# Optimization experiments

Measured on AMD Instinct MI355X. Metric: run time of the kernel, lower is better.

The kernel has to match this reference:

```python
import jax, jax.numpy as jnp
import numpy as np

N, E, G = 50000, 400000, 64   # nodes, edges, graphs
HEADS = 4
F_IN, H1, C3, OUT = 64, 96, 64, 10  # in feats, hidden (3*32), last conv out, classes


def seg_softmax(alpha, index, num_segments):
    # numerically stable softmax over segments (PyG softmax(alpha, edge_index_i))
    amax = jax.ops.segment_max(alpha, index, num_segments)
    amax = jnp.where(jnp.isfinite(amax), amax, 0.0)
    e = jnp.exp(alpha - amax[index])
    denom = jax.ops.segment_sum(e, index, num_segments)
    return e / (denom[index] + 1e-16)


def general_conv(x, src, dst, Wm, bm, att, Ws=None, bs=None):
    # GeneralConv (attention=True, additive, directed_msg, aggr='add')
    C = att.shape[-1]
    m = (x[src] @ Wm + bm).reshape(-1, HEADS, C)              # [E,H,C] gathered messages
    a = jax.nn.leaky_relu((m * att).sum(-1), 0.2)             # [E,H] attention logits
    a = seg_softmax(a, dst, N)                                # segment softmax per dest node
    agg = jax.ops.segment_sum(m * a[..., None], dst, N)       # [N,H,C] scatter-add
    out = agg.mean(axis=1)                                    # head mean -> [N,C]
    if Ws is None:                                            # lin_self = Identity (in==out)
        return out + x
    return out + x @ Ws + bs


def setup_inputs():
    key = jax.random.key(0)
    ks = jax.random.split(key, 16)
    s = 0.05
    return {
        "x": jax.random.normal(ks[0], (N, F_IN), jnp.float32),
        "edge_index": jax.random.randint(ks[1], (2, E), 0, N, jnp.int32),
        "batch": jnp.sort(jax.random.randint(ks[2], (N,), 0, G, jnp.int32)),
        # layer 1: F_IN -> H1
        "Wm1": jax.random.normal(ks[3], (F_IN, HEADS * H1), jnp.float32) * s,
        "bm1": jnp.zeros((HEADS * H1,), jnp.float32),
        "att1": jax.random.normal(ks[4], (HEADS, H1), jnp.float32) * s,
        "Ws1": jax.random.normal(ks[5], (F_IN, H1), jnp.float32) * s,
        "bs1": jnp.zeros((H1,), jnp.float32),
        # layer 2: H1 -> H1 (lin_self = Identity)
        "Wm2": jax.random.normal(ks[6], (H1, HEADS * H1), jnp.float32) * s,
        "bm2": jnp.zeros((HEADS * H1,), jnp.float32),
        "att2": jax.random.normal(ks[7], (HEADS, H1), jnp.float32) * s,
        # layer 3: H1 -> C3
        "Wm3": jax.random.normal(ks[8], (H1, HEADS * C3), jnp.float32) * s,
        "bm3": jnp.zeros((HEADS * C3,), jnp.float32),
        "att3": jax.random.normal(ks[9], (HEADS, C3), jnp.float32) * s,
        "Ws3": jax.random.normal(ks[10], (H1, C3), jnp.float32) * s,
        "bs3": jnp.zeros((C3,), jnp.float32),
        # classifier
        "Wfc": jax.random.normal(ks[11], (C3, OUT), jnp.float32) * s,
        "bfc": jnp.zeros((OUT,), jnp.float32),
    }


def reference(x, edge_index, batch, Wm1, bm1, att1, Ws1, bs1,
              Wm2, bm2, att2, Wm3, bm3, att3, Ws3, bs3, Wfc, bfc):
    src, dst = edge_index[0], edge_index[1]
    h = general_conv(x, src, dst, Wm1, bm1, att1, Ws1, bs1)
    h = general_conv(h, src, dst, Wm2, bm2, att2)
    h = general_conv(h, src, dst, Wm3, bm3, att3, Ws3, bs3)
    # global_mean_pool
    ssum = jax.ops.segment_sum(h, batch, G)
    cnt = jax.ops.segment_sum(jnp.ones((N, 1), h.dtype), batch, G)
    pooled = ssum / jnp.maximum(cnt, 1.0)                      # [G,C3]
    logits = pooled @ Wfc + bfc
    return jax.nn.log_softmax(logits, axis=1)
```

## Files before the change

### kernel.cpp

```cpp
#include <hip/hip_runtime.h>
#include <hip/hip_bf16.h>
#include <stdint.h>

using bf16 = __hip_bfloat16;
typedef __attribute__((ext_vector_type(8))) short bf16x8;
typedef __attribute__((ext_vector_type(4))) float f32x4;
typedef __attribute__((ext_vector_type(2))) float f32x2;

#define NN 50000
#define NE 400000
#define NG 64
#define NHEADS 4
#define FIN 64
#define HID 96
#define CC3 64
#define NOUT 10

#define SCAN_BLOCK 256
#define NPART ((NN + SCAN_BLOCK - 1) / SCAN_BLOCK)
#define GB16 ((NN/16 + 3) / 4)

__device__ __forceinline__ float b2f(bf16 h){ return __bfloat162float(h); }
__device__ __forceinline__ bf16 f2b(float f){ return __float2bfloat16(f); }

#define NTJOBS 5
struct PrepJobs {
  const float* W[NTJOBS]; bf16* WT[NTJOBS]; int K[NTJOBS]; int Nc[NTJOBS];
  const float* LWm[3]; const float* Latt[3]; const float* Lbm[3];
  bf16* LWT[3]; int LK[3]; int LC[3]; int LncMain[3];
  float* lb;
  int* deg; float* psum; int* done;
};
__global__ __launch_bounds__(256) void prep_kernel(PrepJobs j){
  int bid = blockIdx.x;
  if (bid < 3){
    int l = bid;
    const float* Wm = j.LWm[l]; const float* att = j.Latt[l]; const float* bm = j.Lbm[l];
    bf16* WT = j.LWT[l];
    int K = j.LK[l], C = j.LC[l], ncMain = j.LncMain[l];
    for (int idx = threadIdx.x; idx < K*4; idx += 256){
      int k = idx >> 2, h = idx & 3;
      float a = 0.f;
      for (int c=0;c<C;++c) a += Wm[(size_t)k*(4*C) + h*C + c] * att[h*C + c];
      WT[(size_t)(ncMain+h)*K + k] = f2b(a);
    }
    for (int idx = threadIdx.x; idx < 12*K; idx += 256){
      int col = ncMain + 4 + idx / K, k = idx % K;
      WT[(size_t)col*K + k] = f2b(0.f);
    }
    if (threadIdx.x < 4){
      int h = threadIdx.x; float a = 0.f;
      for (int c=0;c<C;++c) a += bm[h*C + c] * att[h*C + c];
      j.lb[l*4 + h] = a;
    }
  } else if (bid < 3 + 256){
    int b = bid - 3;
    for (int t=0; t<NTJOBS; ++t){
      int K = j.K[t], Nc = j.Nc[t], total = K*Nc;
      for (int i = b*256 + threadIdx.x; i < total; i += 256*256){
        int k = i / Nc, n = i % Nc;
        j.WT[t][(size_t)n*K + k] = f2b(j.W[t][i]);
      }
    }
  } else if (bid < 3 + 256 + NPART){
    int i = (bid - 3 - 256)*256 + threadIdx.x;
    if (i < NN) j.deg[i] = 0;
  } else {
    for (int i = threadIdx.x; i < NG*CC3; i += 256) j.psum[i] = 0.f;
    if (threadIdx.x == 0) *j.done = 0;
  }
}

__global__ void deg_kernel(const int* __restrict__ ei, int* __restrict__ deg){
  int e = blockIdx.x*256 + threadIdx.x;
  if (e < NE) atomicAdd(&deg[ei[NE + e]], 1);
}

__global__ __launch_bounds__(256) void scan_part_kernel(const int* __restrict__ deg,
    int* __restrict__ partials, int* __restrict__ done, int* __restrict__ off){
  __shared__ int ws[4];
  __shared__ int lastflag;
  __shared__ int buf[256];
  int i = blockIdx.x*SCAN_BLOCK + threadIdx.x;
  int v = (i < NN) ? deg[i] : 0;
  int lane = threadIdx.x & 63, w = threadIdx.x >> 6;
  int s = v;
  #pragma unroll
  for (int m=1;m<64;m<<=1) s += __shfl_xor(s,m);
  if (lane==0) ws[w]=s;
  __syncthreads();
  if (threadIdx.x==0){
    int tot = ws[0]+ws[1]+ws[2]+ws[3];
    atomicExch(&partials[blockIdx.x], tot);
    __threadfence();
    int old = atomicAdd(done, 1);
    lastflag = (old == NPART-1) ? 1 : 0;
  }
  __syncthreads();
  if (lastflag){
    int t = threadIdx.x;
    int pv = (t < NPART) ? atomicAdd(&partials[t], 0) : 0;
    buf[t] = pv; __syncthreads();
    for (int st=1; st<256; st<<=1){
      int x = (t>=st) ? buf[t-st] : 0;
      __syncthreads();
      buf[t] += x;
      __syncthreads();
    }
    if (t < NPART) atomicExch(&partials[t], buf[t] - pv);
    if (t == 0) off[NN] = buf[255];
  }
}

__global__ __launch_bounds__(256) void scan_final_kernel(const int* __restrict__ deg,
    const int* __restrict__ partials, int* __restrict__ off, int* __restrict__ cursor){
  __shared__ int buf[256];
  int i = blockIdx.x*SCAN_BLOCK + threadIdx.x;
  int t = threadIdx.x;
  int v = (i<NN) ? deg[i] : 0;
  buf[t] = v; __syncthreads();
  for (int s=1;s<256;s<<=1){
    int x = (t>=s) ? buf[t-s] : 0;
    __syncthreads();
    buf[t] += x;
    __syncthreads();
  }
  int ex = partials[blockIdx.x] + buf[t] - v;
  if (i<NN){ off[i]=ex; cursor[i]=ex; }
}

__global__ void scatter_kernel(const int* __restrict__ ei, int* __restrict__ cursor,
                               int* __restrict__ csr_src){
  int e = blockIdx.x*256 + threadIdx.x;
  if (e < NE){
    int d = ei[NE + e];
    int slot = atomicAdd(&cursor[d], 1);
    csr_src[slot] = ei[e];
  }
}

template<int K, bool F32A>
__global__ __launch_bounds__(256) void gemm_mfma(const void* __restrict__ Ap,
    const bf16* __restrict__ WT, const float* __restrict__ biasMain,
    const float* __restrict__ lb4, uint8_t* __restrict__ outMain, int ncMain,
    float* __restrict__ EL, const float* __restrict__ biasSelf,
    bf16* __restrict__ outSelf, int ncSelf, int msgG, int totalU, int UPB)
{
  constexpr int KT = K/32;
  __shared__ unsigned int sbuf[4][16][16];
  const int wave = threadIdx.x >> 6, lane = threadIdx.x & 63;
  const int tile = blockIdx.x*4 + wave;
  if (tile >= NN/16) return;
  const int lm = lane & 15, q = lane >> 4;
  const int nodeRow = tile*16 + lm;
  const int rdRow = lane >> 2, rdCol = lane & 3;
  const int outRow = tile*16 + rdRow;

  bf16x8 xfrag[KT];
  if (F32A){
    const float* Af = (const float*)Ap;
    #pragma unroll
    for (int kt=0; kt<KT; ++kt){
      float4 a0 = *(const float4*)(Af + (size_t)nodeRow*K + kt*32 + q*8);
      float4 a1 = *(const float4*)(Af + (size_t)nodeRow*K + kt*32 + q*8 + 4);
      bf16 tmp[8];
      tmp[0]=f2b(a0.x); tmp[1]=f2b(a0.y); tmp[2]=f2b(a0.z); tmp[3]=f2b(a0.w);
      tmp[4]=f2b(a1.x); tmp[5]=f2b(a1.y); tmp[6]=f2b(a1.z); tmp[7]=f2b(a1.w);
      xfrag[kt] = *(const bf16x8*)tmp;
    }
  } else {
    const bf16* A = (const bf16*)Ap;
    #pragma unroll
    for (int kt=0; kt<KT; ++kt)
      xfrag[kt] = *(const bf16x8*)(A + (size_t)nodeRow*K + kt*32 + q*8);
  }

  const int u0 = blockIdx.y*UPB, u1 = min(u0+UPB, totalU);
  for (int u=u0; u<u1; ++u){
    if (u < msgG){
      #pragma unroll
      for (int t=0;t<4;++t){
        int ct = u*4 + t;
        f32x4 acc = {};
        #pragma unroll
        for (int kt=0; kt<KT; ++kt){
          bf16x8 wfrag = *(const bf16x8*)(WT + (size_t)(ct*16+lm)*K + kt*32 + q*8);
          acc = __builtin_amdgcn_mfma_f32_16x16x32_bf16(wfrag, xfrag[kt], acc, 0,0,0);
        }
        int wc = ct*16 + q*4;
        float v0 = acc[0]+biasMain[wc],   v1 = acc[1]+biasMain[wc+1];
        float v2 = acc[2]+biasMain[wc+2], v3 = acc[3]+biasMain[wc+3];
        int pk = 0;
        pk = __builtin_amdgcn_cvt_pk_fp8_f32(v0, v1, pk, false);
        pk = __builtin_amdgcn_cvt_pk_fp8_f32(v2, v3, pk, true);
        sbuf[wave][lm][t*4 + q] = (unsigned int)pk;
      }
      __builtin_amdgcn_wave_barrier();
      uint4 v = *(uint4*)&sbuf[wave][rdRow][rdCol*4];
      *(uint4*)(outMain + (size_t)outRow*ncMain + u*64 + rdCol*16) = v;
      __builtin_amdgcn_wave_barrier();
    } else if (u == msgG){
      int ct = ncMain/16;
      f32x4 acc = {};
      #pragma unroll
      for (int kt=0; kt<KT; ++kt){
        bf16x8 wfrag = *(const bf16x8*)(WT + (size_t)(ct*16+lm)*K + kt*32 + q*8);
        acc = __builtin_amdgcn_mfma_f32_16x16x32_bf16(wfrag, xfrag[kt], acc, 0,0,0);
      }
      if (q == 0){
        float4 e;
        float l;
        l = acc[0]+lb4[0]; l = (l>=0.f)?l:0.2f*l; e.x = __expf(fminf(fmaxf(l,-60.f),60.f));
        l = acc[1]+lb4[1]; l = (l>=0.f)?l:0.2f*l; e.y = __expf(fminf(fmaxf(l,-60.f),60.f));
        l = acc[2]+lb4[2]; l = (l>=0.f)?l:0.2f*l; e.z = __expf(fminf(fmaxf(l,-60.f),60.f));
        l = acc[3]+lb4[3]; l = (l>=0.f)?l:0.2f*l; e.w = __expf(fminf(fmaxf(l,-60.f),60.f));
        *(float4*)(EL + 4*(size_t)nodeRow) = e;
      }
    } else {
      int sg = u - msgG - 1;
      #pragma unroll
      for (int t=0;t<2;++t){
        int ct = ncMain/16 + 1 + sg*2 + t;
        f32x4 acc = {};
        #pragma unroll
        for (int kt=0; kt<KT; ++kt){
          bf16x8 wfrag = *(const bf16x8*)(WT + (size_t)(ct*16+lm)*K + kt*32 + q*8);
          acc = __builtin_amdgcn_mfma_f32_16x16x32_bf16(wfrag, xfrag[kt], acc, 0,0,0);
        }
        int c = ct*16 + q*4 - ncMain - 16;
        bf16 st[4];
        st[0]=f2b(acc[0]+biasSelf[c]);   st[1]=f2b(acc[1]+biasSelf[c+1]);
        st[2]=f2b(acc[2]+biasSelf[c+2]); st[3]=f2b(acc[3]+biasSelf[c+3]);
        uint2 uu = *(uint2*)st;
        sbuf[wave][lm][t*8 + q*2]     = uu.x;
        sbuf[wave][lm][t*8 + q*2 + 1] = uu.y;
      }
      __builtin_amdgcn_wave_barrier();
      uint4 v = *(uint4*)&sbuf[wave][rdRow][rdCol*4];
      *(uint4*)(outSelf + (size_t)outRow*ncSelf + sg*32 + rdCol*8) = v;
      __builtin_amdgcn_wave_barrier();
    }
  }
}

template<int C, bool FP>
__global__ __launch_bounds__(256) void conv_agg(const int* __restrict__ off,
    const int* __restrict__ csr_src, const float* __restrict__ EL,
    const uint8_t* __restrict__ M8, const bf16* __restrict__ Hself,
    bf16* __restrict__ Hout, const int* __restrict__ batch, float* __restrict__ psum)
{
  constexpr int R = 4*C;
  __shared__ float red[4][R];
  const int wave = threadIdx.x >> 6, lane = threadIdx.x & 63;
  const int n = blockIdx.x*4 + wave;
  const int e0 = off[n], e1 = off[n+1];

  const bool active = (8*lane) < R;
  const int hidx = min(3, (8*lane) / C);
  const int myoff = active ? lane*8 : 0;
  float acc[8] = {0,0,0,0,0,0,0,0};
  float dnl = 0.f;

  for (int base=e0; base<e1; base+=8){
    const int cnt8 = min(8, e1-base);
    int sreg = (lane < cnt8) ? csr_src[base+lane] : 0;
    int sv[8];
    #pragma unroll
    for (int j=0;j<8;++j) sv[j] = __shfl(sreg, j);

    float wl[8]; uint2 u[8];
    #pragma unroll
    for (int j=0;j<8;++j){
      wl[j] = EL[4*(size_t)sv[j] + hidx];
      u[j]  = *(const uint2*)(M8 + (size_t)sv[j]*R + myoff);
    }
    #pragma unroll
    for (int j=0;j<8;++j){
      float w = (j < cnt8) ? wl[j] : 0.f;
      dnl += w;
      f32x2 a0 = __builtin_amdgcn_cvt_pk_f32_fp8((int)u[j].x, false);
      f32x2 a1 = __builtin_amdgcn_cvt_pk_f32_fp8((int)u[j].x, true);
      f32x2 a2 = __builtin_amdgcn_cvt_pk_f32_fp8((int)u[j].y, false);
      f32x2 a3 = __builtin_amdgcn_cvt_pk_f32_fp8((int)u[j].y, true);
      acc[0] += a0.x*w;  acc[1] += a0.y*w;
      acc[2] += a1.x*w;  acc[3] += a1.y*w;
      acc[4] += a2.x*w;  acc[5] += a2.y*w;
      acc[6] += a3.x*w;  acc[7] += a3.y*w;
    }
  }

  float rd = 1.f/(dnl + 1e-16f);
  if (active){
    #pragma unroll
    for (int j=0;j<8;++j) red[wave][8*lane+j] = acc[j]*rd;
  }
  __syncthreads();

  if (!FP){
    for (int c=lane; c<C; c+=64){
      float v = 0.25f*(red[wave][c] + red[wave][C+c] + red[wave][2*C+c] + red[wave][3*C+c]);
      Hout[(size_t)n*C + c] = f2b(v + b2f(Hself[(size_t)n*C + c]));
    }
  } else {
    if (wave == 0){
      int c = lane;
      int nb0 = blockIdx.x*4;
      int curg = batch[nb0];
      float a = 0.f;
      #pragma unroll
      for (int i=0;i<4;++i){
        float v = 0.25f*(red[i][c] + red[i][C+c] + red[i][2*C+c] + red[i][3*C+c]);
        v += b2f(Hself[(size_t)(nb0+i)*C + c]);
        int g = batch[nb0+i];
        if (g != curg){ atomicAdd(&psum[curg*C + c], a); a = 0.f; curg = g; }
        a += v;
      }
      atomicAdd(&psum[curg*C + c], a);
    }
  }
}

__global__ __launch_bounds__(64) void fc_kernel(const float* __restrict__ psum,
    const int* __restrict__ batch, const float* __restrict__ Wfc,
    const float* __restrict__ bfc, float* __restrict__ out){
  int g = blockIdx.x, t = threadIdx.x;
  __shared__ int sb[2];
  if (t < 2){
    int target = g + t;
    int lo=0, hi=NN;
    while (lo<hi){ int mid=(lo+hi)>>1; if (batch[mid]<target) lo=mid+1; else hi=mid; }
    sb[t]=lo;
  }
  __syncthreads();
  float cnt = (float)(sb[1]-sb[0]);
  __shared__ float p[CC3];
  __shared__ float lg[NOUT];
  p[t] = psum[g*CC3 + t] / fmaxf(cnt, 1.0f);
  __syncthreads();
  if (t < NOUT){
    float a = bfc[t];
    for (int c=0;c<CC3;++c) a += p[c]*Wfc[c*NOUT + t];
    lg[t] = a;
  }
  __syncthreads();
  if (t < NOUT){
    float m = -INFINITY;
    #pragma unroll
    for (int i=0;i<NOUT;++i) m = fmaxf(m, lg[i]);
    float s = 0.f;
    #pragma unroll
    for (int i=0;i<NOUT;++i) s += __expf(lg[i]-m);
    out[g*NOUT + t] = lg[t] - m - __logf(s);
  }
}

extern "C" void kernel_launch(void* const* d_in, const int* in_sizes, int n_in,
                              void* d_out, int out_size, void* d_ws, size_t ws_size,
                              hipStream_t stream) {
  const float* xf    = (const float*)d_in[0];
  const int*   ei    = (const int*)d_in[1];
  const int*   batch = (const int*)d_in[2];
  const float* pWm1  = (const float*)d_in[3];
  const float* pbm1  = (const float*)d_in[4];
  const float* patt1 = (const float*)d_in[5];
  const float* pWs1  = (const float*)d_in[6];
  const float* pbs1  = (const float*)d_in[7];
  const float* pWm2  = (const float*)d_in[8];
  const float* pbm2  = (const float*)d_in[9];
  const float* patt2 = (const float*)d_in[10];
  const float* pWm3  = (const float*)d_in[11];
  const float* pbm3  = (const float*)d_in[12];
  const float* patt3 = (const float*)d_in[13];
  const float* pWs3  = (const float*)d_in[14];
  const float* pbs3  = (const float*)d_in[15];
  const float* pWfc  = (const float*)d_in[16];
  const float* pbfc  = (const float*)d_in[17];

  char* p = (char*)d_ws;
  auto alloc = [&](size_t bytes)->char*{ char* q = p; p += (bytes + 255) & ~(size_t)255; return q; };
  int*     deg     = (int*)  alloc(NN*sizeof(int));
  int*     off     = (int*)  alloc((NN+1)*sizeof(int));
  int*     cursor  = (int*)  alloc(NN*sizeof(int));
  int*     csr_src = (int*)  alloc(NE*sizeof(int));
  int*     partials= (int*)  alloc(NPART*sizeof(int));
  int*     done    = (int*)  alloc(sizeof(int));
  float*   EL      = (float*)alloc((size_t)NN*4*sizeof(float));
  uint8_t* Mb8     = (uint8_t*)alloc((size_t)NN*384);
  bf16*    H1b     = (bf16*) alloc((size_t)NN*96*sizeof(bf16));
  bf16*    H2b     = (bf16*) alloc((size_t)NN*96*sizeof(bf16));
  float*   psum    = (float*)alloc((size_t)NG*CC3*sizeof(float));
  bf16*  WT1cat = (bf16*)alloc((size_t)496*FIN*sizeof(bf16));
  bf16*  WT2cat = (bf16*)alloc((size_t)400*HID*sizeof(bf16));
  bf16*  WT3cat = (bf16*)alloc((size_t)336*HID*sizeof(bf16));
  float* lb     = (float*)alloc(12*sizeof(float));
  bf16*  H3b = H1b;

  PrepJobs pj;
  pj.W[0]=pWm1; pj.WT[0]=WT1cat;                 pj.K[0]=FIN; pj.Nc[0]=384;
  pj.W[1]=pWs1; pj.WT[1]=WT1cat+(size_t)400*FIN; pj.K[1]=FIN; pj.Nc[1]=96;
  pj.W[2]=pWm2; pj.WT[2]=WT2cat;                 pj.K[2]=HID; pj.Nc[2]=384;
  pj.W[3]=pWm3; pj.WT[3]=WT3cat;                 pj.K[3]=HID; pj.Nc[3]=256;
  pj.W[4]=pWs3; pj.WT[4]=WT3cat+(size_t)272*HID; pj.K[4]=HID; pj.Nc[4]=64;
  pj.LWm[0]=pWm1; pj.Latt[0]=patt1; pj.Lbm[0]=pbm1; pj.LWT[0]=WT1cat; pj.LK[0]=FIN; pj.LC[0]=96; pj.LncMain[0]=384;
  pj.LWm[1]=pWm2; pj.Latt[1]=patt2; pj.Lbm[1]=pbm2; pj.LWT[1]=WT2cat; pj.LK[1]=HID; pj.LC[1]=96; pj.LncMain[1]=384;
  pj.LWm[2]=pWm3; pj.Latt[2]=patt3; pj.Lbm[2]=pbm3; pj.LWT[2]=WT3cat; pj.LK[2]=HID; pj.LC[2]=64; pj.LncMain[2]=256;
  pj.lb = lb; pj.deg = deg; pj.psum = psum; pj.done = done;
  prep_kernel<<<3+256+NPART+1, 256, 0, stream>>>(pj);

  deg_kernel<<<(NE+255)/256, 256, 0, stream>>>(ei, deg);
  scan_part_kernel<<<NPART, 256, 0, stream>>>(deg, partials, done, off);
  scan_final_kernel<<<NPART, 256, 0, stream>>>(deg, partials, off, cursor);
  scatter_kernel<<<(NE+255)/256, 256, 0, stream>>>(ei, cursor, csr_src);

  const int AB = NN/4;

  gemm_mfma<64,true><<<dim3(GB16,4), 256, 0, stream>>>(xf, WT1cat, pbm1, lb,
                                                       Mb8, 384, EL, pbs1, H1b, 96,
                                                       6, 10, 3);
  conv_agg<96,false><<<AB, 256, 0, stream>>>(off, csr_src, EL, Mb8, H1b, H1b,
                                             batch, psum);
  gemm_mfma<96,false><<<dim3(GB16,4), 256, 0, stream>>>(H1b, WT2cat, pbm2, lb+4,
                                                        Mb8, 384, EL, pbm2, nullptr, 0,
                                                        6, 7, 2);
  conv_agg<96,false><<<AB, 256, 0, stream>>>(off, csr_src, EL, Mb8, H1b, H2b,
                                             batch, psum);
  gemm_mfma<96,false><<<dim3(GB16,3), 256, 0, stream>>>(H2b, WT3cat, pbm3, lb+8,
                                                        Mb8, 256, EL, pbs3, H3b, 64,
                                                        4, 7, 3);
  conv_agg<64,true><<<AB, 256, 0, stream>>>(off, csr_src, EL, Mb8, H3b, nullptr,
                                            batch, psum);

  fc_kernel<<<NG, 64, 0, stream>>>(psum, batch, pWfc, pbfc, (float*)d_out);
}
```

Baseline: 356.2 us.

## Aggregate raw features before the linear map and fuse the GEMM into aggregation

The linear message transform is moved past the attention-weighted aggregation. Each node first gathers bf16 neighbour features per head (4*K wide), and a single per-node GEMM then applies the head-averaged weights, the bias (through an indicator column), the self term, and the next layer's attention logits. This drops the per-layer fp8 message tensor (NN x 384) and the separate GEMM launches, and precomputes folded weight matrices in two prep kernels. The trade-off is a wider gather (bf16 source features per head) and a larger K in the fused GEMM, with rounding now happening at different points.

```diff
diff --git a/kernel.cpp b/kernel.cpp
--- a/kernel.cpp
+++ b/kernel.cpp
@@ -5,12 +5,10 @@
 using bf16 = __hip_bfloat16;
 typedef __attribute__((ext_vector_type(8))) short bf16x8;
 typedef __attribute__((ext_vector_type(4))) float f32x4;
-typedef __attribute__((ext_vector_type(2))) float f32x2;
 
 #define NN 50000
 #define NE 400000
 #define NG 64
-#define NHEADS 4
 #define FIN 64
 #define HID 96
 #define CC3 64
@@ -18,56 +16,105 @@
 
 #define SCAN_BLOCK 256
 #define NPART ((NN + SCAN_BLOCK - 1) / SCAN_BLOCK)
-#define GB16 ((NN/16 + 3) / 4)
 
 __device__ __forceinline__ float b2f(bf16 h){ return __bfloat162float(h); }
 __device__ __forceinline__ bf16 f2b(float f){ return __float2bfloat16(f); }
-
-#define NTJOBS 5
-struct PrepJobs {
-  const float* W[NTJOBS]; bf16* WT[NTJOBS]; int K[NTJOBS]; int Nc[NTJOBS];
-  const float* LWm[3]; const float* Latt[3]; const float* Lbm[3];
-  bf16* LWT[3]; int LK[3]; int LC[3]; int LncMain[3];
-  float* lb;
+__device__ __forceinline__ float bs2f(short s){
+  union { float f; unsigned int u; } c;
+  c.u = ((unsigned int)(unsigned short)s) << 16;
+  return c.f;
+}
+
+struct PrepA {
+  const float *Wm1,*att1,*bm1,*Wm2,*att2,*bm2,*Wm3,*att3,*bm3,*bs1;
+  float *f2,*f3,*lbv,*zb; bf16* WTf1;
   int* deg; float* psum; int* done;
 };
-__global__ __launch_bounds__(256) void prep_kernel(PrepJobs j){
+__global__ __launch_bounds__(256) void prep_a_kernel(PrepA j){
   int bid = blockIdx.x;
-  if (bid < 3){
-    int l = bid;
-    const float* Wm = j.LWm[l]; const float* att = j.Latt[l]; const float* bm = j.Lbm[l];
-    bf16* WT = j.LWT[l];
-    int K = j.LK[l], C = j.LC[l], ncMain = j.LncMain[l];
-    for (int idx = threadIdx.x; idx < K*4; idx += 256){
-      int k = idx >> 2, h = idx & 3;
-      float a = 0.f;
-      for (int c=0;c<C;++c) a += Wm[(size_t)k*(4*C) + h*C + c] * att[h*C + c];
-      WT[(size_t)(ncMain+h)*K + k] = f2b(a);
-    }
-    for (int idx = threadIdx.x; idx < 12*K; idx += 256){
-      int col = ncMain + 4 + idx / K, k = idx % K;
-      WT[(size_t)col*K + k] = f2b(0.f);
-    }
+  if (bid == 0){
+    for (int i=threadIdx.x; i<96*4; i+=256){
+      int k=i>>2, h=i&3; float a=0.f;
+      for (int c=0;c<96;++c) a += j.Wm2[k*384 + h*96 + c]*j.att2[h*96+c];
+      j.f2[i]=a;
+    }
+    for (int i=threadIdx.x; i<96*4; i+=256){
+      int k=i>>2, h=i&3; float a=0.f;
+      for (int c=0;c<64;++c) a += j.Wm3[k*256 + h*64 + c]*j.att3[h*64+c];
+      j.f3[i]=a;
+    }
+    for (int i=threadIdx.x; i<16*64; i+=256){
+      int col=i>>6, k=i&63; float a=0.f;
+      if (col<4){ for (int c=0;c<96;++c) a += j.Wm1[k*384 + col*96 + c]*j.att1[col*96+c]; }
+      j.WTf1[i] = f2b(a);
+    }
+    if (threadIdx.x < 96) j.zb[threadIdx.x] = 0.f;
+    __syncthreads();
     if (threadIdx.x < 4){
-      int h = threadIdx.x; float a = 0.f;
-      for (int c=0;c<C;++c) a += bm[h*C + c] * att[h*C + c];
-      j.lb[l*4 + h] = a;
-    }
-  } else if (bid < 3 + 256){
-    int b = bid - 3;
-    for (int t=0; t<NTJOBS; ++t){
-      int K = j.K[t], Nc = j.Nc[t], total = K*Nc;
-      for (int i = b*256 + threadIdx.x; i < total; i += 256*256){
-        int k = i / Nc, n = i % Nc;
-        j.WT[t][(size_t)n*K + k] = f2b(j.W[t][i]);
-      }
-    }
-  } else if (bid < 3 + 256 + NPART){
-    int i = (bid - 3 - 256)*256 + threadIdx.x;
-    if (i < NN) j.deg[i] = 0;
+      int h = threadIdx.x;
+      float l1=0.f,l2=0.f,l3=0.f;
+      for (int c=0;c<96;++c) l1 += j.bm1[h*96+c]*j.att1[h*96+c];
+      for (int c=0;c<96;++c) l2 += j.bm2[h*96+c]*j.att2[h*96+c];
+      for (int c=0;c<64;++c) l3 += j.bm3[h*64+c]*j.att3[h*64+c];
+      float e2 = l2;
+      for (int k=0;k<96;++k) e2 += j.bs1[k]*j.f2[k*4+h];
+      j.lbv[h]=l1; j.lbv[4+h]=e2; j.lbv[8+h]=l3;
+    }
+  } else if (bid <= NPART){
+    int i=(bid-1)*256+threadIdx.x;
+    if (i<NN) j.deg[i]=0;
   } else {
-    for (int i = threadIdx.x; i < NG*CC3; i += 256) j.psum[i] = 0.f;
-    if (threadIdx.x == 0) *j.done = 0;
+    for (int i=threadIdx.x; i<NG*CC3; i+=256) j.psum[i]=0.f;
+    if (threadIdx.x==0) *j.done = 0;
+  }
+}
+
+struct PrepB {
+  const float *Wm1,*bm1,*Ws1,*Wm2,*bm2,*Wm3,*bm3,*Ws3;
+  const float *f2,*f3;
+  bf16 *WT1,*WT2,*WT3;
+};
+__device__ __forceinline__ float w1full(const PrepB& j, int k, int c){
+  if (k < 256) return 0.25f*j.Wm1[(k&63)*384 + (k>>6)*96 + c];
+  if (k == 256) return 0.25f*(j.bm1[c]+j.bm1[96+c]+j.bm1[192+c]+j.bm1[288+c]);
+  if (k < 288) return 0.f;
+  return j.Ws1[(k-288)*96 + c];
+}
+__device__ __forceinline__ float w2full(const PrepB& j, int k, int c){
+  if (k < 384){ int kk=k%96, h=k/96; return 0.25f*j.Wm2[kk*384 + h*96 + c]; }
+  if (k == 384) return 0.25f*(j.bm2[c]+j.bm2[96+c]+j.bm2[192+c]+j.bm2[288+c]);
+  if (k < 416) return 0.f;
+  return (k-416==c) ? 1.f : 0.f;
+}
+__device__ __forceinline__ float w3full(const PrepB& j, int k, int c){
+  if (k < 384){ int kk=k%96, h=k/96; return 0.25f*j.Wm3[kk*256 + h*64 + c]; }
+  if (k == 384) return 0.25f*(j.bm3[c]+j.bm3[64+c]+j.bm3[128+c]+j.bm3[192+c]);
+  if (k < 416) return 0.f;
+  return j.Ws3[(k-416)*64 + c];
+}
+__global__ __launch_bounds__(256) void prep_b_kernel(PrepB j){
+  int idx = blockIdx.x*256 + threadIdx.x;
+  if (idx < 112*352){
+    int col = idx/352, k = idx - col*352;
+    float v;
+    if (col < 96) v = w1full(j,k,col);
+    else if (col < 100){ int h=col-96; float a=0.f;
+      for (int c=0;c<96;++c) a += w1full(j,k,c)*j.f2[c*4+h]; v=a; }
+    else v = 0.f;
+    j.WT1[col*352 + k] = f2b(v);
+  } else if (idx < 112*352 + 112*512){
+    int r = idx - 112*352;
+    int col = r/512, k = r - col*512;
+    float v;
+    if (col < 96) v = w2full(j,k,col);
+    else if (col < 100){ int h=col-96; float a=0.f;
+      for (int c=0;c<96;++c) a += w2full(j,k,c)*j.f3[c*4+h]; v=a; }
+    else v = 0.f;
+    j.WT2[col*512 + k] = f2b(v);
+  } else {
+    int r = idx - 112*352 - 112*512;
+    int col = r/512, k = r - col*512;
+    j.WT3[col*512 + k] = f2b(w3full(j,k,col));
   }
 }
 
@@ -139,183 +186,171 @@
   }
 }
 
-template<int K, bool F32A>
-__global__ __launch_bounds__(256) void gemm_mfma(const void* __restrict__ Ap,
-    const bf16* __restrict__ WT, const float* __restrict__ biasMain,
-    const float* __restrict__ lb4, uint8_t* __restrict__ outMain, int ncMain,
-    float* __restrict__ EL, const float* __restrict__ biasSelf,
-    bf16* __restrict__ outSelf, int ncSelf, int msgG, int totalU, int UPB)
+__global__ __launch_bounds__(256) void el1_kernel(const float* __restrict__ x,
+    const bf16* __restrict__ WTf1, const float* __restrict__ lbv,
+    bf16* __restrict__ xb, float* __restrict__ EL)
 {
-  constexpr int KT = K/32;
-  __shared__ unsigned int sbuf[4][16][16];
-  const int wave = threadIdx.x >> 6, lane = threadIdx.x & 63;
+  const int wave = threadIdx.x>>6, lane = threadIdx.x&63;
   const int tile = blockIdx.x*4 + wave;
   if (tile >= NN/16) return;
-  const int lm = lane & 15, q = lane >> 4;
-  const int nodeRow = tile*16 + lm;
-  const int rdRow = lane >> 2, rdCol = lane & 3;
-  const int outRow = tile*16 + rdRow;
-
-  bf16x8 xfrag[KT];
-  if (F32A){
-    const float* Af = (const float*)Ap;
+  const int lm = lane&15, q = lane>>4;
+  const size_t row = (size_t)tile*16 + lm;
+  bf16x8 xf[2];
+  #pragma unroll
+  for (int kt=0;kt<2;++kt){
+    float4 a0 = *(const float4*)(x + row*64 + kt*32 + q*8);
+    float4 a1 = *(const float4*)(x + row*64 + kt*32 + q*8 + 4);
+    bf16 t[8] = {f2b(a0.x),f2b(a0.y),f2b(a0.z),f2b(a0.w),
+                 f2b(a1.x),f2b(a1.y),f2b(a1.z),f2b(a1.w)};
+    xf[kt] = *(const bf16x8*)t;
+    *(bf16x8*)(xb + row*64 + kt*32 + q*8) = xf[kt];
+  }
+  f32x4 acc = {};
+  #pragma unroll
+  for (int kt=0;kt<2;++kt){
+    bf16x8 wf = *(const bf16x8*)(WTf1 + (size_t)lm*64 + kt*32 + q*8);
+    acc = __builtin_amdgcn_mfma_f32_16x16x32_bf16(wf, xf[kt], acc, 0,0,0);
+  }
+  if (q==0){
+    float4 e; float l;
+    l=acc[0]+lbv[0]; l=(l>=0.f)?l:0.2f*l; e.x=__expf(fminf(fmaxf(l,-60.f),60.f));
+    l=acc[1]+lbv[1]; l=(l>=0.f)?l:0.2f*l; e.y=__expf(fminf(fmaxf(l,-60.f),60.f));
+    l=acc[2]+lbv[2]; l=(l>=0.f)?l:0.2f*l; e.z=__expf(fminf(fmaxf(l,-60.f),60.f));
+    l=acc[3]+lbv[3]; l=(l>=0.f)?l:0.2f*l; e.w=__expf(fminf(fmaxf(l,-60.f),60.f));
+    *(float4*)(EL + 4*row) = e;
+  }
+}
+
+template<int KH, int NCT, bool POOL>
+__global__ __launch_bounds__(256) void conv_gemm(
+    const int* __restrict__ off, const int* __restrict__ csr_src,
+    const float* __restrict__ ELin, const bf16* __restrict__ Hprev,
+    const bf16* __restrict__ WT, const float* __restrict__ bias,
+    const float* __restrict__ lbe, bf16* __restrict__ Hout,
+    float* __restrict__ ELout, const int* __restrict__ batch,
+    float* __restrict__ psum)
+{
+  constexpr int R   = 4*KH;
+  constexpr int KS  = R + 32;
+  constexpr int KA  = KS + KH;
+  constexpr int KTS = KS/32, KTH = KH/32, KT = KA/32;
+  constexpr int SP  = (KS==288) ? 296 : 424;
+  constexpr int OB  = POOL ? (16*68*4) : (16*104*2);
+  __shared__ __align__(16) unsigned short Slds[16][SP];
+  __shared__ __align__(16) char obuf[OB];
+  __shared__ int sbat[16];
+
+  const int wave = threadIdx.x>>6, lane = threadIdx.x&63;
+  const int n0 = blockIdx.x*16;
+
+  if (POOL && threadIdx.x < 16) sbat[threadIdx.x] = batch[n0+threadIdx.x];
+
+  const bool act = (8*lane) < R;
+  const int h  = min((8*lane)/KH, 3);
+  const int kk = (8*lane) % KH;
+
+  int ofl = 0;
+  if (lane < 5) ofl = off[n0 + wave*4 + lane];
+
+  for (int i=0;i<4;++i){
+    const int e0 = __shfl(ofl, i), e1 = __shfl(ofl, i+1);
+    float acc[8] = {0.f,0.f,0.f,0.f,0.f,0.f,0.f,0.f};
+    float dnl = 0.f;
+    for (int base=e0; base<e1; base+=8){
+      const int cnt = min(8, e1-base);
+      int sreg = (lane < cnt) ? csr_src[base+lane] : 0;
+      int sv[8];
+      #pragma unroll
+      for (int jj=0;jj<8;++jj) sv[jj] = __shfl(sreg, jj);
+      float wl[8]; bf16x8 u[8];
+      #pragma unroll
+      for (int jj=0;jj<8;++jj){
+        wl[jj] = ELin[4*(size_t)sv[jj] + h];
+        u[jj]  = *(const bf16x8*)(Hprev + (size_t)sv[jj]*KH + kk);
+      }
+      #pragma unroll
+      for (int jj=0;jj<8;++jj){
+        float w = (jj < cnt) ? wl[jj] : 0.f;
+        dnl += w;
+        #pragma unroll
+        for (int t=0;t<8;++t) acc[t] += w * bs2f(u[jj][t]);
+      }
+    }
+    const float rd = 1.f/(dnl + 1e-16f);
+    const int srow = wave*4 + i;
+    if (act){
+      bf16 st[8];
+      #pragma unroll
+      for (int t=0;t<8;++t) st[t] = f2b(acc[t]*rd);
+      *(bf16x8*)&Slds[srow][8*lane] = *(const bf16x8*)st;
+    } else if (8*lane < KS){
+      bf16 st[8] = {};
+      if (8*lane == R) st[0] = f2b((e1 > e0) ? 1.f : 0.f);
+      *(bf16x8*)&Slds[srow][8*lane] = *(const bf16x8*)st;
+    }
+  }
+  __syncthreads();
+
+  const int lm = lane&15, q = lane>>4;
+  bf16x8 xf[KT];
+  #pragma unroll
+  for (int kt=0; kt<KTS; ++kt)
+    xf[kt] = *(const bf16x8*)&Slds[lm][kt*32 + q*8];
+  #pragma unroll
+  for (int kt=0; kt<KTH; ++kt)
+    xf[KTS+kt] = *(const bf16x8*)(Hprev + (size_t)(n0+lm)*KH + kt*32 + q*8);
+
+  for (int ct = wave; ct < NCT; ct += 4){
+    f32x4 acc = {};
     #pragma unroll
     for (int kt=0; kt<KT; ++kt){
-      float4 a0 = *(const float4*)(Af + (size_t)nodeRow*K + kt*32 + q*8);
-      float4 a1 = *(const float4*)(Af + (size_t)nodeRow*K + kt*32 + q*8 + 4);
-      bf16 tmp[8];
-      tmp[0]=f2b(a0.x); tmp[1]=f2b(a0.y); tmp[2]=f2b(a0.z); tmp[3]=f2b(a0.w);
-      tmp[4]=f2b(a1.x); tmp[5]=f2b(a1.y); tmp[6]=f2b(a1.z); tmp[7]=f2b(a1.w);
-      xfrag[kt] = *(const bf16x8*)tmp;
-    }
-  } else {
-    const bf16* A = (const bf16*)Ap;
-    #pragma unroll
-    for (int kt=0; kt<KT; ++kt)
-      xfrag[kt] = *(const bf16x8*)(A + (size_t)nodeRow*K + kt*32 + q*8);
-  }
-
-  const int u0 = blockIdx.y*UPB, u1 = min(u0+UPB, totalU);
-  for (int u=u0; u<u1; ++u){
-    if (u < msgG){
-      #pragma unroll
-      for (int t=0;t<4;++t){
-        int ct = u*4 + t;
-        f32x4 acc = {};
-        #pragma unroll
-        for (int kt=0; kt<KT; ++kt){
-          bf16x8 wfrag = *(const bf16x8*)(WT + (size_t)(ct*16+lm)*K + kt*32 + q*8);
-          acc = __builtin_amdgcn_mfma_f32_16x16x32_bf16(wfrag, xfrag[kt], acc, 0,0,0);
-        }
-        int wc = ct*16 + q*4;
-        float v0 = acc[0]+biasMain[wc],   v1 = acc[1]+biasMain[wc+1];
-        float v2 = acc[2]+biasMain[wc+2], v3 = acc[3]+biasMain[wc+3];
-        int pk = 0;
-        pk = __builtin_amdgcn_cvt_pk_fp8_f32(v0, v1, pk, false);
-        pk = __builtin_amdgcn_cvt_pk_fp8_f32(v2, v3, pk, true);
-        sbuf[wave][lm][t*4 + q] = (unsigned int)pk;
-      }
-      __builtin_amdgcn_wave_barrier();
-      uint4 v = *(uint4*)&sbuf[wave][rdRow][rdCol*4];
-      *(uint4*)(outMain + (size_t)outRow*ncMain + u*64 + rdCol*16) = v;
-      __builtin_amdgcn_wave_barrier();
-    } else if (u == msgG){
-      int ct = ncMain/16;
-      f32x4 acc = {};
-      #pragma unroll
-      for (int kt=0; kt<KT; ++kt){
-        bf16x8 wfrag = *(const bf16x8*)(WT + (size_t)(ct*16+lm)*K + kt*32 + q*8);
-        acc = __builtin_amdgcn_mfma_f32_16x16x32_bf16(wfrag, xfrag[kt], acc, 0,0,0);
-      }
+      bf16x8 wf = *(const bf16x8*)(WT + (size_t)(ct*16+lm)*KA + kt*32 + q*8);
+      acc = __builtin_amdgcn_mfma_f32_16x16x32_bf16(wf, xf[kt], acc, 0,0,0);
+    }
+    if (!POOL && ct == NCT-1){
       if (q == 0){
-        float4 e;
-        float l;
-        l = acc[0]+lb4[0]; l = (l>=0.f)?l:0.2f*l; e.x = __expf(fminf(fmaxf(l,-60.f),60.f));
-        l = acc[1]+lb4[1]; l = (l>=0.f)?l:0.2f*l; e.y = __expf(fminf(fmaxf(l,-60.f),60.f));
-        l = acc[2]+lb4[2]; l = (l>=0.f)?l:0.2f*l; e.z = __expf(fminf(fmaxf(l,-60.f),60.f));
-        l = acc[3]+lb4[3]; l = (l>=0.f)?l:0.2f*l; e.w = __expf(fminf(fmaxf(l,-60.f),60.f));
-        *(float4*)(EL + 4*(size_t)nodeRow) = e;
+        float4 e; float l;
+        l=acc[0]+lbe[0]; l=(l>=0.f)?l:0.2f*l; e.x=__expf(fminf(fmaxf(l,-60.f),60.f));
+        l=acc[1]+lbe[1]; l=(l>=0.f)?l:0.2f*l; e.y=__expf(fminf(fmaxf(l,-60.f),60.f));
+        l=acc[2]+lbe[2]; l=(l>=0.f)?l:0.2f*l; e.z=__expf(fminf(fmaxf(l,-60.f),60.f));
+        l=acc[3]+lbe[3]; l=(l>=0.f)?l:0.2f*l; e.w=__expf(fminf(fmaxf(l,-60.f),60.f));
+        *(float4*)(ELout + 4*(size_t)(n0+lm)) = e;
       }
     } else {
-      int sg = u - msgG - 1;
+      const int c = ct*16 + q*4;
+      if (POOL){
+        float* orow = (float*)obuf + lm*68;
+        orow[c]   = acc[0]+bias[c];   orow[c+1] = acc[1]+bias[c+1];
+        orow[c+2] = acc[2]+bias[c+2]; orow[c+3] = acc[3]+bias[c+3];
+      } else {
+        bf16 st[4] = {f2b(acc[0]+bias[c]),   f2b(acc[1]+bias[c+1]),
+                      f2b(acc[2]+bias[c+2]), f2b(acc[3]+bias[c+3])};
+        *(uint2*)((unsigned short*)obuf + lm*104 + c) = *(const uint2*)st;
+      }
+    }
+  }
+  __syncthreads();
+
+  if (!POOL){
+    const int t = threadIdx.x;
+    if (t < 192){
+      const int r = t/12, ch = t - r*12;
+      uint4 v = *(const uint4*)((const unsigned short*)obuf + r*104 + ch*8);
+      *(uint4*)(Hout + (size_t)(n0+r)*96 + ch*8) = v;
+    }
+  } else {
+    if (threadIdx.x < 64){
+      const float* ob = (const float*)obuf;
+      const int c = threadIdx.x;
+      int curg = sbat[0]; float a = 0.f;
       #pragma unroll
-      for (int t=0;t<2;++t){
-        int ct = ncMain/16 + 1 + sg*2 + t;
-        f32x4 acc = {};
-        #pragma unroll
-        for (int kt=0; kt<KT; ++kt){
-          bf16x8 wfrag = *(const bf16x8*)(WT + (size_t)(ct*16+lm)*K + kt*32 + q*8);
-          acc = __builtin_amdgcn_mfma_f32_16x16x32_bf16(wfrag, xfrag[kt], acc, 0,0,0);
-        }
-        int c = ct*16 + q*4 - ncMain - 16;
-        bf16 st[4];
-        st[0]=f2b(acc[0]+biasSelf[c]);   st[1]=f2b(acc[1]+biasSelf[c+1]);
-        st[2]=f2b(acc[2]+biasSelf[c+2]); st[3]=f2b(acc[3]+biasSelf[c+3]);
-        uint2 uu = *(uint2*)st;
-        sbuf[wave][lm][t*8 + q*2]     = uu.x;
-        sbuf[wave][lm][t*8 + q*2 + 1] = uu.y;
-      }
-      __builtin_amdgcn_wave_barrier();
-      uint4 v = *(uint4*)&sbuf[wave][rdRow][rdCol*4];
-      *(uint4*)(outSelf + (size_t)outRow*ncSelf + sg*32 + rdCol*8) = v;
-      __builtin_amdgcn_wave_barrier();
-    }
-  }
-}
-
-template<int C, bool FP>
-__global__ __launch_bounds__(256) void conv_agg(const int* __restrict__ off,
-    const int* __restrict__ csr_src, const float* __restrict__ EL,
-    const uint8_t* __restrict__ M8, const bf16* __restrict__ Hself,
-    bf16* __restrict__ Hout, const int* __restrict__ batch, float* __restrict__ psum)
-{
-  constexpr int R = 4*C;
-  __shared__ float red[4][R];
-  const int wave = threadIdx.x >> 6, lane = threadIdx.x & 63;
-  const int n = blockIdx.x*4 + wave;
-  const int e0 = off[n], e1 = off[n+1];
-
-  const bool active = (8*lane) < R;
-  const int hidx = min(3, (8*lane) / C);
-  const int myoff = active ? lane*8 : 0;
-  float acc[8] = {0,0,0,0,0,0,0,0};
-  float dnl = 0.f;
-
-  for (int base=e0; base<e1; base+=8){
-    const int cnt8 = min(8, e1-base);
-    int sreg = (lane < cnt8) ? csr_src[base+lane] : 0;
-    int sv[8];
-    #pragma unroll
-    for (int j=0;j<8;++j) sv[j] = __shfl(sreg, j);
-
-    float wl[8]; uint2 u[8];
-    #pragma unroll
-    for (int j=0;j<8;++j){
-      wl[j] = EL[4*(size_t)sv[j] + hidx];
-      u[j]  = *(const uint2*)(M8 + (size_t)sv[j]*R + myoff);
-    }
-    #pragma unroll
-    for (int j=0;j<8;++j){
-      float w = (j < cnt8) ? wl[j] : 0.f;
-      dnl += w;
-      f32x2 a0 = __builtin_amdgcn_cvt_pk_f32_fp8((int)u[j].x, false);
-      f32x2 a1 = __builtin_amdgcn_cvt_pk_f32_fp8((int)u[j].x, true);
-      f32x2 a2 = __builtin_amdgcn_cvt_pk_f32_fp8((int)u[j].y, false);
-      f32x2 a3 = __builtin_amdgcn_cvt_pk_f32_fp8((int)u[j].y, true);
-      acc[0] += a0.x*w;  acc[1] += a0.y*w;
-      acc[2] += a1.x*w;  acc[3] += a1.y*w;
-      acc[4] += a2.x*w;  acc[5] += a2.y*w;
-      acc[6] += a3.x*w;  acc[7] += a3.y*w;
-    }
-  }
-
-  float rd = 1.f/(dnl + 1e-16f);
-  if (active){
-    #pragma unroll
-    for (int j=0;j<8;++j) red[wave][8*lane+j] = acc[j]*rd;
-  }
-  __syncthreads();
-
-  if (!FP){
-    for (int c=lane; c<C; c+=64){
-      float v = 0.25f*(red[wave][c] + red[wave][C+c] + red[wave][2*C+c] + red[wave][3*C+c]);
-      Hout[(size_t)n*C + c] = f2b(v + b2f(Hself[(size_t)n*C + c]));
-    }
-  } else {
-    if (wave == 0){
-      int c = lane;
-      int nb0 = blockIdx.x*4;
-      int curg = batch[nb0];
-      float a = 0.f;
-      #pragma unroll
-      for (int i=0;i<4;++i){
-        float v = 0.25f*(red[i][c] + red[i][C+c] + red[i][2*C+c] + red[i][3*C+c]);
-        v += b2f(Hself[(size_t)(nb0+i)*C + c]);
-        int g = batch[nb0+i];
-        if (g != curg){ atomicAdd(&psum[curg*C + c], a); a = 0.f; curg = g; }
+      for (int i=0;i<16;++i){
+        float v = ob[i*68 + c];
+        int g = sbat[i];
+        if (g != curg){ atomicAdd(&psum[curg*64+c], a); a=0.f; curg=g; }
         a += v;
       }
-      atomicAdd(&psum[curg*C + c], a);
+      atomicAdd(&psum[curg*64+c], a);
     }
   }
 }
@@ -384,51 +419,49 @@
   int*     csr_src = (int*)  alloc(NE*sizeof(int));
   int*     partials= (int*)  alloc(NPART*sizeof(int));
   int*     done    = (int*)  alloc(sizeof(int));
-  float*   EL      = (float*)alloc((size_t)NN*4*sizeof(float));
-  uint8_t* Mb8     = (uint8_t*)alloc((size_t)NN*384);
+  float*   ELa     = (float*)alloc((size_t)NN*4*sizeof(float));
+  float*   ELb     = (float*)alloc((size_t)NN*4*sizeof(float));
+  bf16*    xb      = (bf16*) alloc((size_t)NN*64*sizeof(bf16));
   bf16*    H1b     = (bf16*) alloc((size_t)NN*96*sizeof(bf16));
   bf16*    H2b     = (bf16*) alloc((size_t)NN*96*sizeof(bf16));
   float*   psum    = (float*)alloc((size_t)NG*CC3*sizeof(float));
-  bf16*  WT1cat = (bf16*)alloc((size_t)496*FIN*sizeof(bf16));
-  bf16*  WT2cat = (bf16*)alloc((size_t)400*HID*sizeof(bf16));
-  bf16*  WT3cat = (bf16*)alloc((size_t)336*HID*sizeof(bf16));
-  float* lb     = (float*)alloc(12*sizeof(float));
-  bf16*  H3b = H1b;
-
-  PrepJobs pj;
-  pj.W[0]=pWm1; pj.WT[0]=WT1cat;                 pj.K[0]=FIN; pj.Nc[0]=384;
-  pj.W[1]=pWs1; pj.WT[1]=WT1cat+(size_t)400*FIN; pj.K[1]=FIN; pj.Nc[1]=96;
-  pj.W[2]=pWm2; pj.WT[2]=WT2cat;                 pj.K[2]=HID; pj.Nc[2]=384;
-  pj.W[3]=pWm3; pj.WT[3]=WT3cat;                 pj.K[3]=HID; pj.Nc[3]=256;
-  pj.W[4]=pWs3; pj.WT[4]=WT3cat+(size_t)272*HID; pj.K[4]=HID; pj.Nc[4]=64;
-  pj.LWm[0]=pWm1; pj.Latt[0]=patt1; pj.Lbm[0]=pbm1; pj.LWT[0]=WT1cat; pj.LK[0]=FIN; pj.LC[0]=96; pj.LncMain[0]=384;
-  pj.LWm[1]=pWm2; pj.Latt[1]=patt2; pj.Lbm[1]=pbm2; pj.LWT[1]=WT2cat; pj.LK[1]=HID; pj.LC[1]=96; pj.LncMain[1]=384;
-  pj.LWm[2]=pWm3; pj.Latt[2]=patt3; pj.Lbm[2]=pbm3; pj.LWT[2]=WT3cat; pj.LK[2]=HID; pj.LC[2]=64; pj.LncMain[2]=256;
-  pj.lb = lb; pj.deg = deg; pj.psum = psum; pj.done = done;
-  prep_kernel<<<3+256+NPART+1, 256, 0, stream>>>(pj);
+  float*   f2      = (float*)alloc(96*4*sizeof(float));
+  float*   f3      = (float*)alloc(96*4*sizeof(float));
+  float*   lbv     = (float*)alloc(12*sizeof(float));
+  float*   zb      = (float*)alloc(96*sizeof(float));
+  bf16*    WTf1    = (bf16*) alloc((size_t)16*64*sizeof(bf16));
+  bf16*    WT1     = (bf16*) alloc((size_t)112*352*sizeof(bf16));
+  bf16*    WT2     = (bf16*) alloc((size_t)112*512*sizeof(bf16));
+  bf16*    WT3     = (bf16*) alloc((size_t)64*512*sizeof(bf16));
+
+  PrepA pa;
+  pa.Wm1=pWm1; pa.att1=patt1; pa.bm1=pbm1;
+  pa.Wm2=pWm2; pa.att2=patt2; pa.bm2=pbm2;
+  pa.Wm3=pWm3; pa.att3=patt3; pa.bm3=pbm3;
+  pa.bs1=pbs1; pa.f2=f2; pa.f3=f3; pa.lbv=lbv; pa.zb=zb; pa.WTf1=WTf1;
+  pa.deg=deg; pa.psum=psum; pa.done=done;
+  prep_a_kernel<<<NPART+2, 256, 0, stream>>>(pa);
+
+  PrepB pb;
+  pb.Wm1=pWm1; pb.bm1=pbm1; pb.Ws1=pWs1;
+  pb.Wm2=pWm2; pb.bm2=pbm2;
+  pb.Wm3=pWm3; pb.bm3=pbm3; pb.Ws3=pWs3;
+  pb.f2=f2; pb.f3=f3; pb.WT1=WT1; pb.WT2=WT2; pb.WT3=WT3;
+  prep_b_kernel<<<(112*352 + 112*512 + 64*512)/256, 256, 0, stream>>>(pb);
 
   deg_kernel<<<(NE+255)/256, 256, 0, stream>>>(ei, deg);
   scan_part_kernel<<<NPART, 256, 0, stream>>>(deg, partials, done, off);
   scan_final_kernel<<<NPART, 256, 0, stream>>>(deg, partials, off, cursor);
   scatter_kernel<<<(NE+255)/256, 256, 0, stream>>>(ei, cursor, csr_src);
 
-  const int AB = NN/4;
-
-  gemm_mfma<64,true><<<dim3(GB16,4), 256, 0, stream>>>(xf, WT1cat, pbm1, lb,
-                                                       Mb8, 384, EL, pbs1, H1b, 96,
-                                                       6, 10, 3);
-  conv_agg<96,false><<<AB, 256, 0, stream>>>(off, csr_src, EL, Mb8, H1b, H1b,
-                                             batch, psum);
-  gemm_mfma<96,false><<<dim3(GB16,4), 256, 0, stream>>>(H1b, WT2cat, pbm2, lb+4,
-                                                        Mb8, 384, EL, pbm2, nullptr, 0,
-                                                        6, 7, 2);
-  conv_agg<96,false><<<AB, 256, 0, stream>>>(off, csr_src, EL, Mb8, H1b, H2b,
-                                             batch, psum);
-  gemm_mfma<96,false><<<dim3(GB16,3), 256, 0, stream>>>(H2b, WT3cat, pbm3, lb+8,
-                                                        Mb8, 256, EL, pbs3, H3b, 64,
-                                                        4, 7, 3);
-  conv_agg<64,true><<<AB, 256, 0, stream>>>(off, csr_src, EL, Mb8, H3b, nullptr,
-                                            batch, psum);
+  el1_kernel<<<(NN/16+3)/4, 256, 0, stream>>>(xf, WTf1, lbv, xb, ELa);
+
+  conv_gemm<64,7,false><<<NN/16, 256, 0, stream>>>(off, csr_src, ELa, xb,  WT1,
+                                                   pbs1, lbv+4, H1b, ELb, batch, psum);
+  conv_gemm<96,7,false><<<NN/16, 256, 0, stream>>>(off, csr_src, ELb, H1b, WT2,
+                                                   zb,   lbv+8, H2b, ELa, batch, psum);
+  conv_gemm<96,4,true ><<<NN/16, 256, 0, stream>>>(off, csr_src, ELa, H2b, WT3,
+                                                   pbs3, nullptr, nullptr, nullptr, batch, psum);
 
   fc_kernel<<<NG, 64, 0, stream>>>(psum, batch, pWfc, pbfc, (float*)d_out);
 }
```

After: 386.9 us. 1.09x slower.
